# Kernel optimization log

Hardware: AMD Instinct MI355X
Metric: run time of the kernel (lower is better)

The kernel has to match this reference:

```python
import jax, jax.numpy as jnp
import numpy as np

B, N, CS, CZ, CH, H, PQ, PV = 1, 768, 384, 128, 16, 12, 4, 8
INF, EPS = 1e5, 1e-8


def quat_to_rot(q):
    q = q / jnp.linalg.norm(q, axis=-1, keepdims=True)
    w, x, y, z = q[..., 0], q[..., 1], q[..., 2], q[..., 3]
    r0 = jnp.stack([1 - 2 * (y * y + z * z), 2 * (x * y - w * z), 2 * (x * z + w * y)], -1)
    r1 = jnp.stack([2 * (x * y + w * z), 1 - 2 * (x * x + z * z), 2 * (y * z - w * x)], -1)
    r2 = jnp.stack([2 * (x * z - w * y), 2 * (y * z + w * x), 1 - 2 * (x * x + y * y)], -1)
    return jnp.stack([r0, r1, r2], -2)


def setup_inputs() -> dict:
    key = jax.random.key(0)
    ks = jax.random.split(key, 12)
    nrm = lambda k, shp, sc=1.0: jax.random.normal(k, shp, jnp.float32) * sc
    s = nrm(ks[0], (B, N, CS))
    z = nrm(ks[1], (B, N, N, CZ))
    rot = quat_to_rot(nrm(ks[2], (B, N, 4)))
    trans = nrm(ks[3], (B, N, 3))
    mask = jnp.ones((B, N), jnp.float32)
    dout = H * (CZ + CH + PV * 4)
    return dict(
        s=s, z=z, rot=rot, trans=trans, mask=mask,
        w_q=nrm(ks[4], (H * CH, CS), 0.02), b_q=jnp.zeros((H * CH,), jnp.float32),
        w_kv=nrm(ks[5], (2 * H * CH, CS), 0.02), b_kv=jnp.zeros((2 * H * CH,), jnp.float32),
        w_qp=nrm(ks[6], (H * PQ * 3, CS), 0.02), b_qp=jnp.zeros((H * PQ * 3,), jnp.float32),
        w_kvp=nrm(ks[7], (H * (PQ + PV) * 3, CS), 0.02), b_kvp=jnp.zeros((H * (PQ + PV) * 3,), jnp.float32),
        w_b=nrm(ks[8], (H, CZ), 0.02), b_b=jnp.zeros((H,), jnp.float32),
        head_weights=jnp.full((H,), 0.541324854612918, jnp.float32),
        w_out=nrm(ks[9], (CS, dout), 0.02), b_out=jnp.zeros((CS,), jnp.float32),
    )


def ipa_forward(s, z, rot, trans, mask, w_q, b_q, w_kv, b_kv, w_qp, b_qp,
                w_kvp, b_kvp, w_b, b_b, head_weights, w_out, b_out):
    # scalar q/k/v: [B,N,H,CH]
    q = (s @ w_q.T + b_q).reshape(B, N, H, CH)
    kv = (s @ w_kv.T + b_kv).reshape(B, N, H, 2 * CH)
    k, v = kv[..., :CH], kv[..., CH:]
    # point projections in local frame, then rigid apply: x_glob = R x + t
    qp = (s @ w_qp.T + b_qp).reshape(B, N, H, PQ, 3)
    kvp = (s @ w_kvp.T + b_kvp).reshape(B, N, H, PQ + PV, 3)
    t = trans[:, :, None, None, :]
    q_pts = jnp.einsum('bnij,bnhpj->bnhpi', rot, qp) + t
    kv_pts = jnp.einsum('bnij,bnhpj->bnhpi', rot, kvp) + t
    k_pts, v_pts = kv_pts[..., :PQ, :], kv_pts[..., PQ:, :]
    # pair bias: [B,H,N,N]
    b = jnp.moveaxis(z @ w_b.T + b_b, -1, 1)
    # scalar attention logits
    a = jnp.einsum('bihc,bjhc->bhij', q, k) * np.sqrt(1.0 / (3 * CH))
    a = a + np.sqrt(1.0 / 3) * b
    # point-distance attention: [B,N,N,H]
    diff = q_pts[:, :, None] - k_pts[:, None]  # [B,N,N,H,PQ,3]
    d2 = jnp.sum(diff * diff, axis=-1)  # [B,N,N,H,PQ]
    hw = jax.nn.softplus(head_weights) * np.sqrt(1.0 / (3 * (PQ * 9.0 / 2)))
    pt_att = -0.5 * jnp.sum(d2 * hw[None, None, None, :, None], axis=-1)
    a = a + jnp.moveaxis(pt_att, -1, 1)
    # mask
    sq_mask = INF * (mask[:, :, None] * mask[:, None, :] - 1.0)  # [B,N,N]
    a = jax.nn.softmax(a + sq_mask[:, None], axis=-1)  # [B,H,N,N]
    # outputs
    o = jnp.einsum('bhij,bjhc->bihc', a, v).reshape(B, N, H * CH)
    o_pt = jnp.einsum('bhij,bjhpx->bihpx', a, v_pts)  # global frame
    o_pt_loc = jnp.einsum('bnji,bnhpj->bnhpi', rot, o_pt - t)  # R^T (x - t)
    o_pt_norm = jnp.sqrt(jnp.sum(o_pt_loc * o_pt_loc, axis=-1) + EPS)  # [B,N,H,PV]
    o_pair = jnp.einsum('bhij,bijc->bihc', a, z).reshape(B, N, H * CZ)
    cat = jnp.concatenate([o, o_pt_loc.reshape(B, N, H * PV * 3),
                           o_pt_norm.reshape(B, N, H * PV), o_pair], axis=-1)
    return cat @ w_out.T + b_out  # [B,N,CS]


def reference(s, z, rot, trans, mask, w_q, b_q, w_kv, b_kv, w_qp, b_qp,
              w_kvp, b_kvp, w_b, b_b, head_weights, w_out, b_out):
    return ipa_forward(s, z, rot, trans, mask, w_q, b_q, w_kv, b_kv, w_qp, b_qp,
                       w_kvp, b_kvp, w_b, b_b, head_weights, w_out, b_out)
```

## Files before the change

kernel.cpp:

```cpp
#include <hip/hip_runtime.h>
#include <math.h>

#define Nn 768
#define NN 589824
#define DOUT 2112

#define WS_Q   0
#define WS_K   147456
#define WS_QP  442368
#define WS_KP  552960
#define WS_CAT 884736
#define WS_A   2506752
#define WS_VT  6045696

typedef unsigned short u16;
typedef unsigned int u32;

using bf16x8 = __attribute__((ext_vector_type(8))) short;
using f32x4  = __attribute__((ext_vector_type(4))) float;

__device__ __forceinline__ float bf2f(u16 u) {
  union { float f; u32 i; } x; x.i = ((u32)u) << 16; return x.f;
}
__device__ __forceinline__ u16 f2bf(float f) {
  union { float f; u32 i; } x; x.f = f;
  u32 r = x.i + 0x7FFFu + ((x.i >> 16) & 1u);
  return (u16)(r >> 16);
}

__global__ __launch_bounds__(256) void k_proj(
    const float* __restrict__ s, const float* __restrict__ rot, const float* __restrict__ trans,
    const float* __restrict__ w_q, const float* __restrict__ b_q,
    const float* __restrict__ w_kv, const float* __restrict__ b_kv,
    const float* __restrict__ w_qp, const float* __restrict__ b_qp,
    const float* __restrict__ w_kvp, const float* __restrict__ b_kvp,
    float* __restrict__ ws)
{
  __shared__ float s16[16][384];
  __shared__ float praw[16][192];
  __shared__ float rot16[16][9];
  __shared__ float t16[16][3];
  const int t = threadIdx.x;
  const int ib = blockIdx.x, fg = blockIdx.y;
  const int i0 = ib * 16;
  u16* VT = (u16*)(ws + WS_VT);

  {
    const float4* sp = (const float4*)(s + (size_t)i0 * 384);
    float4* dp = (float4*)&s16[0][0];
    for (int idx = t; idx < 1536; idx += 256) dp[idx] = sp[idx];
  }
  if (fg >= 3) {
    if (t < 144) rot16[t / 9][t % 9] = rot[i0 * 9 + t];
    else if (t < 192) { int g = t - 144; t16[g / 3][g % 3] = trans[i0 * 3 + g]; }
  }
  __syncthreads();

  const int rg = t >> 6;
  const int fl = t & 63;
  for (int p = 0; p < 3; p++) {
    const int f_loc = p * 64 + fl;
    const int F = fg * 192 + f_loc;
    const float* wrow; float bias;
    if (F < 192)      { wrow = w_q   + (size_t)F * 384;          bias = b_q[F]; }
    else if (F < 576) { int g = F - 192; wrow = w_kv  + (size_t)g * 384; bias = b_kv[g]; }
    else if (F < 720) { int g = F - 576; wrow = w_qp  + (size_t)g * 384; bias = b_qp[g]; }
    else              { int g = F - 720; wrow = w_kvp + (size_t)g * 384; bias = b_kvp[g]; }
    float a0 = bias, a1 = bias, a2 = bias, a3 = bias;
    const float4* w4 = (const float4*)wrow;
    #pragma unroll 4
    for (int c4 = 0; c4 < 96; c4++) {
      float4 wv = w4[c4];
      const float4 v0 = *(const float4*)&s16[rg * 4 + 0][c4 * 4];
      const float4 v1 = *(const float4*)&s16[rg * 4 + 1][c4 * 4];
      const float4 v2 = *(const float4*)&s16[rg * 4 + 2][c4 * 4];
      const float4 v3 = *(const float4*)&s16[rg * 4 + 3][c4 * 4];
      a0 += wv.x * v0.x + wv.y * v0.y + wv.z * v0.z + wv.w * v0.w;
      a1 += wv.x * v1.x + wv.y * v1.y + wv.z * v1.z + wv.w * v1.w;
      a2 += wv.x * v2.x + wv.y * v2.y + wv.z * v2.z + wv.w * v2.w;
      a3 += wv.x * v3.x + wv.y * v3.y + wv.z * v3.z + wv.w * v3.w;
    }
    float av[4] = {a0, a1, a2, a3};
    if (F < 576) {
      if (F < 192) {
        float* base = ws + WS_Q + ((F >> 4) * Nn) * 16 + (F & 15);
        #pragma unroll
        for (int r = 0; r < 4; r++) base[(i0 + rg * 4 + r) * 16] = av[r];
      } else {
        int g = F - 192, hh = g >> 5, x = g & 31;
        if (x < 16) {
          float* base = ws + WS_K + (hh * Nn) * 16 + x;
          #pragma unroll
          for (int r = 0; r < 4; r++) base[(i0 + rg * 4 + r) * 16] = av[r];
        } else {
          u16* vt = VT + (size_t)(hh * 40 + (x - 16)) * 768;
          #pragma unroll
          for (int r = 0; r < 4; r++) vt[i0 + rg * 4 + r] = f2bf(av[r]);
        }
      }
    } else {
      #pragma unroll
      for (int r = 0; r < 4; r++) praw[rg * 4 + r][f_loc] = av[r];
    }
  }
  if (fg >= 3) {
    __syncthreads();
    #pragma unroll
    for (int k = 0; k < 4; k++) {
      int tk = t + k * 256;
      int row = tk >> 6, tri = tk & 63;
      int g3 = tri * 3;
      int i = i0 + row;
      float vx = praw[row][g3], vy = praw[row][g3 + 1], vz = praw[row][g3 + 2];
      const float* R = rot16[row];
      const float* T = t16[row];
      float o0 = R[0] * vx + R[1] * vy + R[2] * vz + T[0];
      float o1 = R[3] * vx + R[4] * vy + R[5] * vz + T[1];
      float o2 = R[6] * vx + R[7] * vy + R[8] * vz + T[2];
      int pt_g = (fg - 3) * 192 + g3;
      if (pt_g < 144) {
        int hh = pt_g / 12, pp = (pt_g / 3) & 3;
        float* dst = ws + WS_QP + (hh * Nn + i) * 12 + pp * 3;
        dst[0] = o0; dst[1] = o1; dst[2] = o2;
      } else {
        int gg = pt_g - 144; int hh = gg / 36, pp = (gg / 3) % 12;
        if (pp < 4) {
          float* dst = ws + WS_KP + (hh * Nn + i) * 12 + pp * 3;
          dst[0] = o0; dst[1] = o1; dst[2] = o2;
        } else {
          u16* vt = VT + (size_t)(hh * 40 + 16 + (pp - 4) * 3) * 768 + i;
          vt[0] = f2bf(o0); vt[768] = f2bf(o1); vt[1536] = f2bf(o2);
        }
      }
    }
  }
}

__global__ __launch_bounds__(256) void k_bias(
    const float* __restrict__ z, const float* __restrict__ w_b, const float* __restrict__ b_b,
    u16* __restrict__ A)
{
  __shared__ float wb[12][128];
  __shared__ float bb[12];
  const int t = threadIdx.x;
  for (int idx = t; idx < 1536; idx += 256) wb[idx >> 7][idx & 127] = w_b[idx];
  if (t < 12) bb[t] = b_b[t];
  __syncthreads();
  const size_t pair = (size_t)blockIdx.x * 256 + t;
  const float4* zp = (const float4*)(z + pair * 128);
  float acc[12];
  #pragma unroll
  for (int h = 0; h < 12; h++) acc[h] = 0.f;
  #pragma unroll 4
  for (int c4 = 0; c4 < 32; c4++) {
    float4 zv = zp[c4];
    #pragma unroll
    for (int h = 0; h < 12; h++) {
      const float4 wv = *(const float4*)&wb[h][c4 * 4];
      acc[h] += zv.x * wv.x + zv.y * wv.y + zv.z * wv.z + zv.w * wv.w;
    }
  }
  #pragma unroll
  for (int h = 0; h < 12; h++) A[(size_t)h * NN + pair] = f2bf(acc[h] + bb[h]);
}

__global__ __launch_bounds__(256) void k_attn(
    const float* __restrict__ ws, u16* __restrict__ A,
    const float* __restrict__ mask, const float* __restrict__ head_weights)
{
  const int h = blockIdx.x;
  const int i0 = blockIdx.y * 4;
  const int t = threadIdx.x;
  const int lane = t & 63, wv = t >> 6;
  __shared__ float qrow[4][16];
  __shared__ float qp4[4][12];
  __shared__ float mi4[4];
  __shared__ float red[4][4];
  __shared__ float Msh[4], Ssh[4];

  if (t < 64) { int r = t >> 4, c = t & 15; qrow[r][c] = ws[WS_Q + (h * Nn + i0 + r) * 16 + c]; }
  else if (t < 112) { int g = t - 64; int r = g / 12, d = g - r * 12; qp4[r][d] = ws[WS_QP + (h * Nn + i0 + r) * 12 + d]; }
  else if (t < 116) mi4[t - 112] = mask[i0 + t - 112];
  const float hw = log1pf(__expf(head_weights[h]));
  const float cpt = -0.5f * hw * 0.13608276348795434f;
  __syncthreads();

  float L[4][3];
  float lmax[4] = {-1e30f, -1e30f, -1e30f, -1e30f};
  #pragma unroll
  for (int jj = 0; jj < 3; jj++) {
    const int j = t + jj * 256;
    const float4* kp = (const float4*)(ws + WS_K + (size_t)(h * Nn + j) * 16);
    float kr[16];
    #pragma unroll
    for (int u = 0; u < 4; u++) { float4 vv = kp[u]; kr[u*4] = vv.x; kr[u*4+1] = vv.y; kr[u*4+2] = vv.z; kr[u*4+3] = vv.w; }
    const float4* pp4 = (const float4*)(ws + WS_KP + (size_t)(h * Nn + j) * 12);
    float kpt[12];
    #pragma unroll
    for (int u = 0; u < 3; u++) { float4 vv = pp4[u]; kpt[u*4] = vv.x; kpt[u*4+1] = vv.y; kpt[u*4+2] = vv.z; kpt[u*4+3] = vv.w; }
    const float mj = mask[j];
    #pragma unroll
    for (int r = 0; r < 4; r++) {
      float qk = 0.f;
      #pragma unroll
      for (int c = 0; c < 16; c++) qk += qrow[r][c] * kr[c];
      float d2 = 0.f;
      #pragma unroll
      for (int d = 0; d < 12; d++) { float df = qp4[r][d] - kpt[d]; d2 += df * df; }
      float bias = bf2f(A[h * NN + (i0 + r) * Nn + j]);
      float Lv = qk * 0.14433756729740643f + 0.57735026918962584f * bias + cpt * d2
               + 100000.0f * (mi4[r] * mj - 1.0f);
      L[r][jj] = Lv;
      lmax[r] = fmaxf(lmax[r], Lv);
    }
  }
  #pragma unroll
  for (int r = 0; r < 4; r++) {
    float v = lmax[r];
    #pragma unroll
    for (int o = 32; o > 0; o >>= 1) v = fmaxf(v, __shfl_xor(v, o));
    if (lane == 0) red[wv][r] = v;
  }
  __syncthreads();
  if (t < 4) Msh[t] = fmaxf(fmaxf(red[0][t], red[1][t]), fmaxf(red[2][t], red[3][t]));
  __syncthreads();
  float lsum[4] = {0.f, 0.f, 0.f, 0.f};
  #pragma unroll
  for (int jj = 0; jj < 3; jj++) {
    #pragma unroll
    for (int r = 0; r < 4; r++) {
      float e = __expf(L[r][jj] - Msh[r]);
      L[r][jj] = e; lsum[r] += e;
    }
  }
  #pragma unroll
  for (int r = 0; r < 4; r++) {
    float v = lsum[r];
    #pragma unroll
    for (int o = 32; o > 0; o >>= 1) v += __shfl_xor(v, o);
    if (lane == 0) red[wv][r] = v;
  }
  __syncthreads();
  if (t < 4) Ssh[t] = red[0][t] + red[1][t] + red[2][t] + red[3][t];
  __syncthreads();
  float inv[4];
  #pragma unroll
  for (int r = 0; r < 4; r++) inv[r] = 1.0f / Ssh[r];
  #pragma unroll
  for (int jj = 0; jj < 3; jj++) {
    int j = t + jj * 256;
    #pragma unroll
    for (int r = 0; r < 4; r++)
      A[h * NN + (i0 + r) * Nn + j] = f2bf(L[r][jj] * inv[r]);
  }
}

__global__ __launch_bounds__(192) void k_out_ov(
    const u16* __restrict__ A, const u16* __restrict__ VT,
    const float* __restrict__ rot, const float* __restrict__ trans,
    float* __restrict__ ws)
{
  const int ib = blockIdx.x, h = blockIdx.y;
  const int i0 = ib * 16;
  const int t = threadIdx.x;
  const int w = t >> 6, lane = t & 63;
  const int n = lane & 15, quad = lane >> 4;
  __shared__ float opt[16][26];

  const int col40 = w * 16 + n;
  const bool bvalid = col40 < 40;
  const u16* abase = A + (size_t)h * NN + (size_t)(i0 + n) * Nn + quad * 8;
  const u16* bbase = VT + (size_t)(h * 40 + (bvalid ? col40 : 0)) * 768 + quad * 8;

  f32x4 acc = {0.f, 0.f, 0.f, 0.f};
  #pragma unroll 4
  for (int kk = 0; kk < 24; kk++) {
    bf16x8 af = *(const bf16x8*)(abase + kk * 32);
    bf16x8 bf = *(const bf16x8*)(bbase + kk * 32);
    if (!bvalid) bf = bf16x8{0, 0, 0, 0, 0, 0, 0, 0};
    acc = __builtin_amdgcn_mfma_f32_16x16x32_bf16(af, bf, acc, 0, 0, 0);
  }

  const int mrow = quad * 4;
  if (w == 0) {
    float* cb = ws + WS_CAT + (size_t)i0 * DOUT + h * 16 + n;
    #pragma unroll
    for (int r = 0; r < 4; r++) cb[(size_t)(mrow + r) * DOUT] = acc[r];
  } else if (w == 1 || n < 8) {
    const int col = (w - 1) * 16 + n;
    #pragma unroll
    for (int r = 0; r < 4; r++) opt[mrow + r][col] = acc[r];
  }
  __syncthreads();
  if (t < 128) {
    const int ii = t >> 3, p = t & 7;
    const int i = i0 + ii;
    float R[9], T[3];
    #pragma unroll
    for (int u = 0; u < 9; u++) R[u] = rot[i * 9 + u];
    #pragma unroll
    for (int u = 0; u < 3; u++) T[u] = trans[i * 3 + u];
    float g0 = opt[ii][p * 3 + 0] - T[0];
    float g1 = opt[ii][p * 3 + 1] - T[1];
    float g2 = opt[ii][p * 3 + 2] - T[2];
    float lx = R[0] * g0 + R[3] * g1 + R[6] * g2;
    float ly = R[1] * g0 + R[4] * g1 + R[7] * g2;
    float lz = R[2] * g0 + R[5] * g1 + R[8] * g2;
    float* cb = ws + WS_CAT + (size_t)i * DOUT;
    cb[192 + (h * 8 + p) * 3 + 0] = lx;
    cb[192 + (h * 8 + p) * 3 + 1] = ly;
    cb[192 + (h * 8 + p) * 3 + 2] = lz;
    cb[480 + h * 8 + p] = sqrtf(lx * lx + ly * ly + lz * lz + 1e-8f);
  }
}

__global__ __launch_bounds__(256) void k_out_pair(
    const float* __restrict__ z, const u16* __restrict__ A, float* __restrict__ ws)
{
  const int i = blockIdx.x;
  const int t = threadIdx.x;
  __shared__ u16 aL[12 * 768];
  __shared__ float zch[16][128];
  __shared__ float af[12][16];
  const int c = t & 127, grp = t >> 7;

  for (int idx = t; idx < 4608; idx += 256) {
    int hh = idx / 384, u = idx - hh * 384;
    ((u32*)aL)[hh * 384 + u] = ((const u32*)(A + (size_t)hh * NN + i * Nn))[u];
  }
  float acc[6];
  #pragma unroll
  for (int hh = 0; hh < 6; hh++) acc[hh] = 0.f;

  const float4* zsrc = (const float4*)(z + (size_t)i * Nn * 128);
  float4 p0 = zsrc[t], p1 = zsrc[t + 256];

  for (int jb = 0; jb < 48; jb++) {
    __syncthreads();
    {
      int i0x = t, i1x = t + 256;
      *(float4*)&zch[i0x >> 5][(i0x & 31) * 4] = p0;
      *(float4*)&zch[i1x >> 5][(i1x & 31) * 4] = p1;
    }
    if (t < 192) af[t >> 4][t & 15] = bf2f(aL[(t >> 4) * 768 + jb * 16 + (t & 15)]);
    __syncthreads();
    if (jb + 1 < 48) {
      const float4* zn = zsrc + (size_t)(jb + 1) * 512;
      p0 = zn[t]; p1 = zn[t + 256];
    }
    #pragma unroll 4
    for (int r = 0; r < 16; r++) {
      float zv = zch[r][c];
      #pragma unroll
      for (int hh = 0; hh < 6; hh++)
        acc[hh] += af[grp * 6 + hh][r] * zv;
    }
  }
  float* cb = ws + WS_CAT + (size_t)i * DOUT + 576;
  #pragma unroll
  for (int hh = 0; hh < 6; hh++)
    cb[(grp * 6 + hh) * 128 + c] = acc[hh];
}

__global__ __launch_bounds__(256) void k_final(
    const float* __restrict__ ws, const float* __restrict__ w_out, const float* __restrict__ b_out,
    float* __restrict__ outp)
{
  const int i0 = blockIdx.x * 16, c0 = blockIdx.y * 32;
  const int t = threadIdx.x;
  const int ci = t & 31, ig = t >> 5;
  __shared__ float wch[32][65];
  __shared__ float cch[16][64];
  float acc0 = 0.f, acc1 = 0.f;
  for (int dc = 0; dc < 33; dc++) {
    __syncthreads();
    #pragma unroll
    for (int k = 0; k < 8; k++) {
      int idx = t + k * 256;
      int r = idx >> 6, u = idx & 63;
      wch[r][u] = w_out[(size_t)(c0 + r) * DOUT + dc * 64 + u];
    }
    #pragma unroll
    for (int k = 0; k < 4; k++) {
      int idx = t + k * 256;
      int r = idx >> 6, u = idx & 63;
      cch[r][u] = ws[WS_CAT + (size_t)(i0 + r) * DOUT + dc * 64 + u];
    }
    __syncthreads();
    #pragma unroll 8
    for (int d = 0; d < 64; d++) {
      float w = wch[ci][d];
      acc0 += cch[ig][d] * w;
      acc1 += cch[ig + 8][d] * w;
    }
  }
  float bo = b_out[c0 + ci];
  outp[(size_t)(i0 + ig) * 384 + c0 + ci]     = acc0 + bo;
  outp[(size_t)(i0 + ig + 8) * 384 + c0 + ci] = acc1 + bo;
}

extern "C" void kernel_launch(void* const* d_in, const int* in_sizes, int n_in,
                              void* d_out, int out_size, void* d_ws, size_t ws_size,
                              hipStream_t stream)
{
  const float* s      = (const float*)d_in[0];
  const float* z      = (const float*)d_in[1];
  const float* rot    = (const float*)d_in[2];
  const float* trans  = (const float*)d_in[3];
  const float* mask   = (const float*)d_in[4];
  const float* w_q    = (const float*)d_in[5];
  const float* b_q    = (const float*)d_in[6];
  const float* w_kv   = (const float*)d_in[7];
  const float* b_kv   = (const float*)d_in[8];
  const float* w_qp   = (const float*)d_in[9];
  const float* b_qp   = (const float*)d_in[10];
  const float* w_kvp  = (const float*)d_in[11];
  const float* b_kvp  = (const float*)d_in[12];
  const float* w_b    = (const float*)d_in[13];
  const float* b_b    = (const float*)d_in[14];
  const float* hwts   = (const float*)d_in[15];
  const float* w_out  = (const float*)d_in[16];
  const float* b_out  = (const float*)d_in[17];
  float* ws = (float*)d_ws;
  u16* A = (u16*)(ws + WS_A);
  u16* VT = (u16*)(ws + WS_VT);
  float* outp = (float*)d_out;

  k_proj<<<dim3(48, 6), dim3(256), 0, stream>>>(s, rot, trans, w_q, b_q, w_kv, b_kv,
                                                w_qp, b_qp, w_kvp, b_kvp, ws);
  k_bias<<<dim3(2304), dim3(256), 0, stream>>>(z, w_b, b_b, A);
  k_attn<<<dim3(12, 192), dim3(256), 0, stream>>>(ws, A, mask, hwts);
  k_out_ov<<<dim3(48, 12), dim3(192), 0, stream>>>(A, VT, rot, trans, ws);
  k_out_pair<<<dim3(768), dim3(256), 0, stream>>>(z, A, ws);
  k_final<<<dim3(48, 12), dim3(256), 0, stream>>>(ws, w_out, b_out, outp);
}
```

Measured before the change: 799.8 us.

## Run output projection on bf16 MFMA with split hi/lo precision

The fp32 concat buffer and w_out are now stored as bf16 high and low parts. A new conversion kernel splits w_out on every call. The final projection runs as a split-K MFMA kernel using three bf16 products (hh, hl, lh), reduced across four waves through shared memory. This replaces the scalar fp32 LDS GEMM with matrix cores, at the cost of an extra launch, extra conversion work, and slightly reduced precision.

```diff
diff --git a/kernel.cpp b/kernel.cpp
--- a/kernel.cpp
+++ b/kernel.cpp
@@ -9,9 +9,12 @@
 #define WS_K   147456
 #define WS_QP  442368
 #define WS_KP  552960
-#define WS_CAT 884736
 #define WS_A   2506752
 #define WS_VT  6045696
+#define WS_CH  6230016
+#define WS_CL  7041024
+#define WS_WH  7852032
+#define WS_WL  8257536
 
 typedef unsigned short u16;
 typedef unsigned int u32;
@@ -26,6 +29,11 @@
   union { float f; u32 i; } x; x.f = f;
   u32 r = x.i + 0x7FFFu + ((x.i >> 16) & 1u);
   return (u16)(r >> 16);
+}
+__device__ __forceinline__ void wr_hl(u16* ch, u16* cl, int idx, float v) {
+  u16 hb = f2bf(v);
+  ch[idx] = hb;
+  cl[idx] = f2bf(v - bf2f(hb));
 }
 
 __global__ __launch_bounds__(256) void k_proj(
@@ -266,6 +274,8 @@
   const int w = t >> 6, lane = t & 63;
   const int n = lane & 15, quad = lane >> 4;
   __shared__ float opt[16][26];
+  u16* CH = (u16*)(ws + WS_CH);
+  u16* CL = (u16*)(ws + WS_CL);
 
   const int col40 = w * 16 + n;
   const bool bvalid = col40 < 40;
@@ -283,9 +293,10 @@
 
   const int mrow = quad * 4;
   if (w == 0) {
-    float* cb = ws + WS_CAT + (size_t)i0 * DOUT + h * 16 + n;
-    #pragma unroll
-    for (int r = 0; r < 4; r++) cb[(size_t)(mrow + r) * DOUT] = acc[r];
+    u16* chb = CH + (size_t)i0 * DOUT + h * 16 + n;
+    u16* clb = CL + (size_t)i0 * DOUT + h * 16 + n;
+    #pragma unroll
+    for (int r = 0; r < 4; r++) wr_hl(chb, clb, (mrow + r) * DOUT, acc[r]);
   } else if (w == 1 || n < 8) {
     const int col = (w - 1) * 16 + n;
     #pragma unroll
@@ -306,11 +317,12 @@
     float lx = R[0] * g0 + R[3] * g1 + R[6] * g2;
     float ly = R[1] * g0 + R[4] * g1 + R[7] * g2;
     float lz = R[2] * g0 + R[5] * g1 + R[8] * g2;
-    float* cb = ws + WS_CAT + (size_t)i * DOUT;
-    cb[192 + (h * 8 + p) * 3 + 0] = lx;
-    cb[192 + (h * 8 + p) * 3 + 1] = ly;
-    cb[192 + (h * 8 + p) * 3 + 2] = lz;
-    cb[480 + h * 8 + p] = sqrtf(lx * lx + ly * ly + lz * lz + 1e-8f);
+    u16* chb = CH + (size_t)i * DOUT;
+    u16* clb = CL + (size_t)i * DOUT;
+    wr_hl(chb, clb, 192 + (h * 8 + p) * 3 + 0, lx);
+    wr_hl(chb, clb, 192 + (h * 8 + p) * 3 + 1, ly);
+    wr_hl(chb, clb, 192 + (h * 8 + p) * 3 + 2, lz);
+    wr_hl(chb, clb, 480 + h * 8 + p, sqrtf(lx * lx + ly * ly + lz * lz + 1e-8f));
   }
 }
 
@@ -356,47 +368,68 @@
         acc[hh] += af[grp * 6 + hh][r] * zv;
     }
   }
-  float* cb = ws + WS_CAT + (size_t)i * DOUT + 576;
+  u16* chb = (u16*)(ws + WS_CH) + (size_t)i * DOUT + 576;
+  u16* clb = (u16*)(ws + WS_CL) + (size_t)i * DOUT + 576;
   #pragma unroll
   for (int hh = 0; hh < 6; hh++)
-    cb[(grp * 6 + hh) * 128 + c] = acc[hh];
-}
-
-__global__ __launch_bounds__(256) void k_final(
-    const float* __restrict__ ws, const float* __restrict__ w_out, const float* __restrict__ b_out,
-    float* __restrict__ outp)
-{
-  const int i0 = blockIdx.x * 16, c0 = blockIdx.y * 32;
-  const int t = threadIdx.x;
-  const int ci = t & 31, ig = t >> 5;
-  __shared__ float wch[32][65];
-  __shared__ float cch[16][64];
-  float acc0 = 0.f, acc1 = 0.f;
-  for (int dc = 0; dc < 33; dc++) {
-    __syncthreads();
-    #pragma unroll
-    for (int k = 0; k < 8; k++) {
-      int idx = t + k * 256;
-      int r = idx >> 6, u = idx & 63;
-      wch[r][u] = w_out[(size_t)(c0 + r) * DOUT + dc * 64 + u];
-    }
-    #pragma unroll
-    for (int k = 0; k < 4; k++) {
-      int idx = t + k * 256;
-      int r = idx >> 6, u = idx & 63;
-      cch[r][u] = ws[WS_CAT + (size_t)(i0 + r) * DOUT + dc * 64 + u];
-    }
-    __syncthreads();
-    #pragma unroll 8
-    for (int d = 0; d < 64; d++) {
-      float w = wch[ci][d];
-      acc0 += cch[ig][d] * w;
-      acc1 += cch[ig + 8][d] * w;
-    }
-  }
-  float bo = b_out[c0 + ci];
-  outp[(size_t)(i0 + ig) * 384 + c0 + ci]     = acc0 + bo;
-  outp[(size_t)(i0 + ig + 8) * 384 + c0 + ci] = acc1 + bo;
+    wr_hl(chb, clb, (grp * 6 + hh) * 128 + c, acc[hh]);
+}
+
+__global__ __launch_bounds__(256) void k_wcvt(const float* __restrict__ w_out, float* __restrict__ ws)
+{
+  const int idx = blockIdx.x * 256 + threadIdx.x;
+  float4 v = ((const float4*)w_out)[idx];
+  u16 h0 = f2bf(v.x), h1 = f2bf(v.y), h2 = f2bf(v.z), h3 = f2bf(v.w);
+  ushort4 hv; hv.x = h0; hv.y = h1; hv.z = h2; hv.w = h3;
+  ushort4 lv;
+  lv.x = f2bf(v.x - bf2f(h0));
+  lv.y = f2bf(v.y - bf2f(h1));
+  lv.z = f2bf(v.z - bf2f(h2));
+  lv.w = f2bf(v.w - bf2f(h3));
+  ((ushort4*)(ws + WS_WH))[idx] = hv;
+  ((ushort4*)(ws + WS_WL))[idx] = lv;
+}
+
+__global__ __launch_bounds__(256) void k_final_mfma(
+    const float* __restrict__ ws, const float* __restrict__ b_out, float* __restrict__ outp)
+{
+  const int i0 = blockIdx.x * 16, c0 = blockIdx.y * 16;
+  const int t = threadIdx.x;
+  const int w = t >> 6, lane = t & 63;
+  const int n = lane & 15, quad = lane >> 4;
+  const u16* CH  = (const u16*)(ws + WS_CH);
+  const u16* CL  = (const u16*)(ws + WS_CL);
+  const u16* WHp = (const u16*)(ws + WS_WH);
+  const u16* WLp = (const u16*)(ws + WS_WL);
+  const u16* ah_p = CH  + (size_t)(i0 + n) * DOUT + quad * 8;
+  const u16* al_p = CL  + (size_t)(i0 + n) * DOUT + quad * 8;
+  const u16* bh_p = WHp + (size_t)(c0 + n) * DOUT + quad * 8;
+  const u16* bl_p = WLp + (size_t)(c0 + n) * DOUT + quad * 8;
+
+  const int s0 = (w * 66) >> 2, s1 = ((w + 1) * 66) >> 2;
+  f32x4 acc = {0.f, 0.f, 0.f, 0.f};
+  for (int ss = s0; ss < s1; ss++) {
+    bf16x8 ah = *(const bf16x8*)(ah_p + ss * 32);
+    bf16x8 al = *(const bf16x8*)(al_p + ss * 32);
+    bf16x8 bh = *(const bf16x8*)(bh_p + ss * 32);
+    bf16x8 bl = *(const bf16x8*)(bl_p + ss * 32);
+    acc = __builtin_amdgcn_mfma_f32_16x16x32_bf16(ah, bh, acc, 0, 0, 0);
+    acc = __builtin_amdgcn_mfma_f32_16x16x32_bf16(ah, bl, acc, 0, 0, 0);
+    acc = __builtin_amdgcn_mfma_f32_16x16x32_bf16(al, bh, acc, 0, 0, 0);
+  }
+
+  __shared__ float red[4][64][4];
+  #pragma unroll
+  for (int r = 0; r < 4; r++) red[w][lane][r] = acc[r];
+  __syncthreads();
+  if (w == 0) {
+    const float bo = b_out[c0 + n];
+    #pragma unroll
+    for (int r = 0; r < 4; r++) {
+      float v = red[0][lane][r] + red[1][lane][r] + red[2][lane][r] + red[3][lane][r] + bo;
+      outp[(size_t)(i0 + quad * 4 + r) * 384 + c0 + n] = v;
+    }
+  }
 }
 
 extern "C" void kernel_launch(void* const* d_in, const int* in_sizes, int n_in,
@@ -426,11 +459,12 @@
   u16* VT = (u16*)(ws + WS_VT);
   float* outp = (float*)d_out;
 
+  k_wcvt<<<dim3(792), dim3(256), 0, stream>>>(w_out, ws);
   k_proj<<<dim3(48, 6), dim3(256), 0, stream>>>(s, rot, trans, w_q, b_q, w_kv, b_kv,
                                                 w_qp, b_qp, w_kvp, b_kvp, ws);
   k_bias<<<dim3(2304), dim3(256), 0, stream>>>(z, w_b, b_b, A);
   k_attn<<<dim3(12, 192), dim3(256), 0, stream>>>(ws, A, mask, hwts);
   k_out_ov<<<dim3(48, 12), dim3(192), 0, stream>>>(A, VT, rot, trans, ws);
   k_out_pair<<<dim3(768), dim3(256), 0, stream>>>(z, A, ws);
-  k_final<<<dim3(48, 12), dim3(256), 0, stream>>>(ws, w_out, b_out, outp);
-}
+  k_final_mfma<<<dim3(48, 24), dim3(256), 0, stream>>>(ws, b_out, outp);
+}
```

Result: faster. 669.7 us (-16.3%).
